# Kernel tuning notes

Measured on AMD Instinct MI355X. Metric: run time of the kernel, lower is better.

Reference implementation:

```python
import jax, jax.numpy as jnp
import numpy as np

V_PER_MESH = 6596
HIDDEN = 128
# per-body-part clamp limits from the original module (parts 1..14)
LIMITS = jnp.array([0.04, 0.06, 0.04, 0.04, 0.02, 0.02, 0.04, 0.04,
                    0.03, 0.03, 0.02, 0.02, 0.01, 0.01], dtype=jnp.float32)


def setup_inputs() -> dict:
    key = jax.random.key(0)
    ks = jax.random.split(key, 16)
    B, V, H = 32, V_PER_MESH, HIDDEN
    N = B * V
    E = 3 * N
    inp = {}
    inp["verts"] = jax.random.normal(ks[0], (N, 3), jnp.float32)
    inp["normals"] = jax.random.normal(ks[1], (N, 3), jnp.float32)
    inp["anchor_v"] = jax.random.uniform(ks[2], (V, 3), jnp.float32)
    inp["edges"] = jax.random.randint(ks[3], (E, 2), 0, N)
    inp["part_id"] = jax.random.randint(ks[4], (V,), 0, 14)
    dims = [3, H + 3, H + 3]  # first gconv sees only vert normals (vert_feat_dim=0)
    i = 5
    for l, d in enumerate(dims):
        s = 1.0 / np.sqrt(d)
        inp[f"w0_{l}"] = jax.random.normal(ks[i], (d, H), jnp.float32) * s; i += 1
        inp[f"b0_{l}"] = jnp.zeros((H,), jnp.float32)
        inp[f"w1_{l}"] = jax.random.normal(ks[i], (d, H), jnp.float32) * s; i += 1
        inp[f"b1_{l}"] = jnp.zeros((H,), jnp.float32)
    inp["w_off"] = jax.random.normal(ks[i], (H + 3, 3), jnp.float32) * 0.01
    inp["b_off"] = jnp.zeros((3,), jnp.float32)
    return inp


def _forward(verts, normals, anchor_v, edges, part_id, layers, w_off, b_off):
    N = verts.shape[0]
    B = N // V_PER_MESH
    e0, e1 = edges[:, 0], edges[:, 1]
    feats = normals  # vert_pos_packed (verts_normals_packed), vert_feats=None
    for (w0, b0, w1, b1) in layers:
        x0 = feats @ w0 + b0            # [N,H] self transform
        x1 = feats @ w1 + b1            # [N,H] neighbor transform
        # undirected gather-scatter over mesh edges
        nbr = jnp.zeros_like(x0).at[e0].add(x1[e1]).at[e1].add(x1[e0])
        h = jax.nn.relu(x0 + nbr)       # vert_feats_nopos
        feats = jnp.concatenate([h, normals], axis=1)  # [N,H+3]
    deform = jnp.tanh(feats @ w_off + b_off)  # [N,3]
    # per-body-part clamp, vectorized: one limit per vertex, tiled over meshes
    lim = jnp.tile(LIMITS[part_id], B)[:, None]          # [N,1]
    clamped = jnp.clip(deform, -lim, lim)
    anchor = jnp.tile(anchor_v, (B, 1))                  # [N,3]
    new_verts = verts + clamped * anchor                 # offset_verts
    return new_verts, h


def reference(verts, normals, anchor_v, edges, part_id,
              w0_0, b0_0, w1_0, b1_0,
              w0_1, b0_1, w1_1, b1_1,
              w0_2, b0_2, w1_2, b1_2,
              w_off, b_off):
    layers = [(w0_0, b0_0, w1_0, b1_0),
              (w0_1, b0_1, w1_1, b1_1),
              (w0_2, b0_2, w1_2, b1_2)]
    return _forward(verts, normals, anchor_v, edges, part_id, layers, w_off, b_off)
```

## Files before the change

### kernel.cpp

```cpp
#include <hip/hip_runtime.h>

#define N_TOT 211072
#define V_MESH 6596
#define E_TOT 633216
#define CAP 32
#define KD 264
#define KSTEPS 8

typedef __attribute__((ext_vector_type(8))) short bf16x8;
typedef __attribute__((ext_vector_type(4))) float f32x4;

__constant__ float c_LIM[14] = {0.04f,0.06f,0.04f,0.04f,0.02f,0.02f,0.04f,0.04f,
                                0.03f,0.03f,0.02f,0.02f,0.01f,0.01f};

__device__ __forceinline__ unsigned f2bf(float f) {
    unsigned x = __float_as_uint(f);
    return (x + 0x7fffu + ((x >> 16) & 1u)) >> 16;
}
__device__ __forceinline__ float bflo(unsigned u) { return __uint_as_float(u << 16); }
__device__ __forceinline__ float bfhi(unsigned u) { return __uint_as_float(u & 0xffff0000u); }
__device__ __forceinline__ unsigned cvt_pk_bf16(float lo, float hi) {
    unsigned r;
    asm("v_cvt_pk_bf16_f32 %0, %1, %2" : "=v"(r) : "v"(lo), "v"(hi));
    return r;
}

__global__ __launch_bounds__(256) void fill_adj_kernel(const int* __restrict__ edges,
                                                       int* __restrict__ cnt,
                                                       int* __restrict__ adj) {
    int e = blockIdx.x * 256 + threadIdx.x;
    if (e >= E_TOT) return;
    int2 ed = ((const int2*)edges)[e];
    int p0 = atomicAdd(&cnt[ed.x], 1);
    if (p0 < CAP) adj[(size_t)ed.x * CAP + p0] = ed.y;
    int p1 = atomicAdd(&cnt[ed.y], 1);
    if (p1 < CAP) adj[(size_t)ed.y * CAP + p1] = ed.x;
}

__global__ __launch_bounds__(256) void prep_nrm4_kernel(const float* __restrict__ normals,
                                                        float4* __restrict__ nrm4) {
    int i = blockIdx.x * 256 + threadIdx.x;
    if (i >= N_TOT) return;
    float4 v;
    v.x = normals[(size_t)i * 3 + 0];
    v.y = normals[(size_t)i * 3 + 1];
    v.z = normals[(size_t)i * 3 + 2];
    v.w = 0.f;
    nrm4[i] = v;
}

__global__ __launch_bounds__(256) void nsum_kernel(const float4* __restrict__ nrm4,
                                                   const int* __restrict__ cnt,
                                                   const int* __restrict__ adj,
                                                   float4* __restrict__ SS) {
    int i = blockIdx.x * 256 + threadIdx.x;
    if (i >= N_TOT) return;
    int deg = cnt[i]; if (deg > CAP) deg = CAP;
    const int4* a4 = (const int4*)(adj + (size_t)i * CAP);
    int4 A = a4[0], B = a4[1];
    float4 n0 = nrm4[A.x], n1 = nrm4[A.y], n2 = nrm4[A.z], n3 = nrm4[A.w];
    float4 m0 = nrm4[B.x], m1 = nrm4[B.y], m2 = nrm4[B.z], m3 = nrm4[B.w];
    float sx = ((n0.x + n1.x) + (n2.x + n3.x)) + ((m0.x + m1.x) + (m2.x + m3.x));
    float sy = ((n0.y + n1.y) + (n2.y + n3.y)) + ((m0.y + m1.y) + (m2.y + m3.y));
    float sz = ((n0.z + n1.z) + (n2.z + n3.z)) + ((m0.z + m1.z) + (m2.z + m3.z));
    for (int bq = 8; bq < deg; bq += 8) {
        int4 C = a4[bq / 4], D = a4[bq / 4 + 1];
        float4 p0 = nrm4[C.x], p1 = nrm4[C.y], p2 = nrm4[C.z], p3 = nrm4[C.w];
        float4 q0 = nrm4[D.x], q1 = nrm4[D.y], q2 = nrm4[D.z], q3 = nrm4[D.w];
        sx += ((p0.x + p1.x) + (p2.x + p3.x)) + ((q0.x + q1.x) + (q2.x + q3.x));
        sy += ((p0.y + p1.y) + (p2.y + p3.y)) + ((q0.y + q1.y) + (q2.y + q3.y));
        sz += ((p0.z + p1.z) + (p2.z + p3.z)) + ((q0.z + q1.z) + (q2.z + q3.z));
    }
    float4 out; out.x = sx; out.y = sy; out.z = sz; out.w = (float)deg;
    SS[i] = out;
}

__global__ __launch_bounds__(256) void conv_w2_kernel(const float* __restrict__ w0,
                                                      const float* __restrict__ b0,
                                                      const float* __restrict__ w1,
                                                      const float* __restrict__ b1,
                                                      short* __restrict__ Wt,
                                                      float4* __restrict__ hdA,
                                                      float4* __restrict__ hdB) {
    int c = blockIdx.x;
    for (int k = threadIdx.x; k < KD; k += 256) {
        unsigned val = 0u;
        if (k < 128)      val = f2bf(w0[(size_t)k * 128 + c]);
        else if (k < 256) val = f2bf(w1[(size_t)(k - 128) * 128 + c]);
        Wt[(size_t)c * KD + k] = (short)val;
    }
    if (threadIdx.x == 0) {
        hdA[c] = make_float4(b0[c], b1[c], w0[128 * 128 + c], w0[129 * 128 + c]);
        hdB[c] = make_float4(w0[130 * 128 + c], w1[128 * 128 + c],
                             w1[129 * 128 + c], w1[130 * 128 + c]);
    }
}

__global__ __launch_bounds__(1024) void fused1_kernel(const float4* __restrict__ nrm4,
                                                      const float4* __restrict__ SS,
                                                      const float* __restrict__ w0,
                                                      const float* __restrict__ b0,
                                                      const float* __restrict__ w1,
                                                      const float* __restrict__ b1,
                                                      unsigned* __restrict__ hout) {
    __shared__ float wL[2][3][128];
    __shared__ float bL[2][128];
    int tid  = threadIdx.x;
    int w    = tid >> 6;
    int lane = tid & 63;
    int i    = blockIdx.x * 16 + w;

    if (tid < 768) {
        int mm = tid / 384, r = tid - mm * 384;
        (&wL[mm][0][0])[r] = (mm ? w1 : w0)[r];
    } else if (tid < 1024) {
        int t2 = tid - 768;
        if (t2 < 256) bL[t2 >> 7][t2 & 127] = ((t2 >> 7) ? b1 : b0)[t2 & 127];
    }
    float4 self4 = nrm4[i];
    float4 S4 = SS[i];
    float degf = S4.w;
    __syncthreads();

    int c0 = 2 * lane, c1 = 2 * lane + 1;
    float h0 = bL[0][c0] + degf * bL[1][c0]
             + self4.x * wL[0][0][c0] + self4.y * wL[0][1][c0] + self4.z * wL[0][2][c0]
             + S4.x * wL[1][0][c0] + S4.y * wL[1][1][c0] + S4.z * wL[1][2][c0];
    float h1 = bL[0][c1] + degf * bL[1][c1]
             + self4.x * wL[0][0][c1] + self4.y * wL[0][1][c1] + self4.z * wL[0][2][c1]
             + S4.x * wL[1][0][c1] + S4.y * wL[1][1][c1] + S4.z * wL[1][2][c1];
    hout[(size_t)i * 64 + lane] = cvt_pk_bf16(fmaxf(h0, 0.f), fmaxf(h1, 0.f));
}

template<int LAST>
__global__ __launch_bounds__(512, 6) void fused2_kernel(const unsigned* __restrict__ hin,
                                                        const float4* __restrict__ nrm4,
                                                        const float4* __restrict__ SS,
                                                        const int* __restrict__ cnt,
                                                        const int* __restrict__ adj,
                                                        const short* __restrict__ Wt,
                                                        const float4* __restrict__ hdA,
                                                        const float4* __restrict__ hdB,
                                                        unsigned* __restrict__ hnext,
                                                        const float* __restrict__ verts,
                                                        const float* __restrict__ anchor_v,
                                                        const int* __restrict__ part_id,
                                                        const float* __restrict__ w_off,
                                                        const float* __restrict__ b_off,
                                                        float* __restrict__ houtf,
                                                        float* __restrict__ out_verts) {
    __shared__ short tileA[16 * KD];
    __shared__ unsigned tileC[16 * 64];
    __shared__ float headL[16][8];
    __shared__ float woL[131 * 3];
    __shared__ float partL[8][16][3];

    int tid  = threadIdx.x;
    int w    = tid >> 6;
    int lane = tid & 63;
    int g    = lane >> 4;
    int ln   = lane & 15;
    int row0 = blockIdx.x * 16;
    int rA   = 2 * w, rB = 2 * w + 1;
    int iA   = row0 + rA, iB = row0 + rB;

    if (LAST) {
        for (int t = tid; t < 131 * 3; t += 512) woL[t] = w_off[t];
    }

    int node = (lane < 32) ? iA : iB;
    int jv = adj[(size_t)node * CAP + (lane & 31)];
    int degA = cnt[iA]; degA = (degA > CAP) ? CAP : degA;
    int degB = cnt[iB]; degB = (degB > CAP) ? CAP : degB;
    unsigned selfA = hin[(size_t)iA * 64 + lane];
    unsigned selfB = hin[(size_t)iB * 64 + lane];
    float4 nn = nrm4[node];
    float4 sv = SS[node];
    if ((lane & 31) == 0) {
        int r = rA + (lane >> 5);
        headL[r][0] = nn.x; headL[r][1] = nn.y; headL[r][2] = nn.z; headL[r][3] = sv.w;
        headL[r][4] = sv.x; headL[r][5] = sv.y; headL[r][6] = sv.z; headL[r][7] = 0.f;
    }

    const unsigned* hb = hin + lane;
    unsigned uA[16], uB[16];
    #pragma unroll
    for (int q = 0; q < 16; ++q) {
        int jA = __builtin_amdgcn_readlane(jv, q);
        uA[q] = hb[(ptrdiff_t)jA * 64];
    }
    #pragma unroll
    for (int q = 0; q < 16; ++q) {
        int jB = __builtin_amdgcn_readlane(jv, 32 + q);
        uB[q] = hb[(ptrdiff_t)jB * 64];
    }
    float sA0 = 0.f, sA1 = 0.f, sB0 = 0.f, sB1 = 0.f;
    #pragma unroll
    for (int q = 0; q < 16; ++q) { sA0 += bflo(uA[q]); sA1 += bfhi(uA[q]); }
    #pragma unroll
    for (int q = 0; q < 16; ++q) { sB0 += bflo(uB[q]); sB1 += bfhi(uB[q]); }

    degA = __builtin_amdgcn_readfirstlane(degA);
    degB = __builtin_amdgcn_readfirstlane(degB);
    int degM = (degA > degB) ? degA : degB;
    for (int bq = 16; bq < degM; bq += 8) {
        unsigned vA[8], vB[8];
        #pragma unroll
        for (int q = 0; q < 8; ++q) {
            int jA = __builtin_amdgcn_readlane(jv, bq + q);
            int jB = __builtin_amdgcn_readlane(jv, 32 + bq + q);
            vA[q] = hb[(ptrdiff_t)jA * 64];
            vB[q] = hb[(ptrdiff_t)jB * 64];
        }
        #pragma unroll
        for (int q = 0; q < 8; ++q) {
            sA0 += bflo(vA[q]); sA1 += bfhi(vA[q]);
            sB0 += bflo(vB[q]); sB1 += bfhi(vB[q]);
        }
    }

    unsigned* tA = (unsigned*)tileA;
    tA[rA * 132 + lane]      = selfA;
    tA[rB * 132 + lane]      = selfB;
    tA[rA * 132 + 64 + lane] = cvt_pk_bf16(sA0, sA1);
    tA[rB * 132 + 64 + lane] = cvt_pk_bf16(sB0, sB1);
    if (lane < 4) {
        tA[rA * 132 + 128 + lane] = 0u;
        tA[rB * 132 + 128 + lane] = 0u;
    }

    int cb = w * 16, c = cb + ln;
    bf16x8 bfrag[KSTEPS];
    #pragma unroll
    for (int kk = 0; kk < KSTEPS; ++kk)
        bfrag[kk] = *(const bf16x8*)(Wt + (size_t)c * KD + kk * 32 + g * 8);
    float4 hA = hdA[c], hB = hdB[c];
    __syncthreads();

    f32x4 acc;
    #pragma unroll
    for (int j = 0; j < 4; ++j) {
        int r = g * 4 + j;
        acc[j] = hA.x + headL[r][3] * hA.y
               + headL[r][0] * hA.z + headL[r][1] * hA.w + headL[r][2] * hB.x
               + headL[r][4] * hB.y + headL[r][5] * hB.z + headL[r][6] * hB.w;
    }
    #pragma unroll
    for (int kk = 0; kk < KSTEPS; ++kk) {
        bf16x8 af = *(const bf16x8*)(tileA + ln * KD + kk * 32 + g * 8);
        acc = __builtin_amdgcn_mfma_f32_16x16x32_bf16(af, bfrag[kk], acc, 0, 0, 0);
    }
    #pragma unroll
    for (int j = 0; j < 4; ++j) acc[j] = fmaxf(acc[j], 0.f);

    if (!LAST) {
        #pragma unroll
        for (int j = 0; j < 4; ++j) {
            float po = __shfl_xor(acc[j], 1);
            if (!(ln & 1)) {
                unsigned pk = cvt_pk_bf16(acc[j], po);
                int r = g * 4 + j;
                int d = (cb + ln) >> 1;
                tileC[r * 64 + (d ^ ((r & 12) << 1))] = pk;
            }
        }
        __syncthreads();
        int r2 = 2 * w + (lane >> 5);
        int d2 = (lane & 31) * 2;
        int key = (r2 & 12) << 1;
        uint2 v2 = *(const uint2*)&tileC[r2 * 64 + (d2 ^ key)];
        *(uint2*)(hnext + (size_t)(row0 + r2) * 64 + d2) = v2;
    } else {
        #pragma unroll
        for (int j = 0; j < 4; ++j) {
            int r = g * 4 + j;
            float p0 = acc[j] * woL[c * 3 + 0];
            float p1 = acc[j] * woL[c * 3 + 1];
            float p2 = acc[j] * woL[c * 3 + 2];
            #pragma unroll
            for (int d = 1; d < 16; d <<= 1) {
                p0 += __shfl_xor(p0, d);
                p1 += __shfl_xor(p1, d);
                p2 += __shfl_xor(p2, d);
            }
            if (ln == 0) {
                partL[w][r][0] = p0; partL[w][r][1] = p1; partL[w][r][2] = p2;
            }
        }
        __syncthreads();
        float* tCf = (float*)tileA;
        #pragma unroll
        for (int j = 0; j < 4; ++j) {
            int r = g * 4 + j;
            tCf[r * 132 + c] = acc[j];
        }
        __syncthreads();
        {
            int r = tid >> 5, c4 = (tid & 31) * 4;
            float4 v = *(const float4*)&tCf[r * 132 + c4];
            *(float4*)(houtf + (size_t)(row0 + r) * 128 + c4) = v;
        }
        if (tid < 48) {
            int r = tid / 3, t = tid - r * 3;
            int i = row0 + r;
            float s = 0.f;
            #pragma unroll
            for (int ww = 0; ww < 8; ++ww) s += partL[ww][r][t];
            s += headL[r][0] * woL[128 * 3 + t] + headL[r][1] * woL[129 * 3 + t]
               + headL[r][2] * woL[130 * 3 + t] + b_off[t];
            float dd = tanhf(s);
            int v = i % V_MESH;
            float lim = c_LIM[part_id[v]];
            dd = fminf(fmaxf(dd, -lim), lim);
            out_verts[(size_t)i * 3 + t] =
                verts[(size_t)i * 3 + t] + dd * anchor_v[(size_t)v * 3 + t];
        }
    }
}

extern "C" void kernel_launch(void* const* d_in, const int* in_sizes, int n_in,
                              void* d_out, int out_size, void* d_ws, size_t ws_size,
                              hipStream_t stream) {
    const float* verts    = (const float*)d_in[0];
    const float* normals  = (const float*)d_in[1];
    const float* anchor_v = (const float*)d_in[2];
    const int*   edges    = (const int*)d_in[3];
    const int*   part_id  = (const int*)d_in[4];
    const float* w0_0 = (const float*)d_in[5];
    const float* b0_0 = (const float*)d_in[6];
    const float* w1_0 = (const float*)d_in[7];
    const float* b1_0 = (const float*)d_in[8];
    const float* w0_1 = (const float*)d_in[9];
    const float* b0_1 = (const float*)d_in[10];
    const float* w1_1 = (const float*)d_in[11];
    const float* b1_1 = (const float*)d_in[12];
    const float* w0_2 = (const float*)d_in[13];
    const float* b0_2 = (const float*)d_in[14];
    const float* w1_2 = (const float*)d_in[15];
    const float* b1_2 = (const float*)d_in[16];
    const float* w_off = (const float*)d_in[17];
    const float* b_off = (const float*)d_in[18];

    float* out_verts = (float*)d_out;
    float* houtf = (float*)d_out + (size_t)3 * N_TOT;

    char* p = (char*)d_ws;
    unsigned* h1b = (unsigned*)p;  p += (size_t)(N_TOT + 1) * 64 * 4;
    unsigned* h2b = (unsigned*)p;  p += (size_t)(N_TOT + 1) * 64 * 4;
    int*    cnt  = (int*)p;        p += (size_t)N_TOT * 4;
    int*    adj  = (int*)p;        p += (size_t)N_TOT * CAP * 4;
    short*  Wt1  = (short*)p;      p += 128 * KD * 2;
    short*  Wt2  = (short*)p;      p += 128 * KD * 2;
    float4* hdA1 = (float4*)p;     p += 128 * 16;
    float4* hdB1 = (float4*)p;     p += 128 * 16;
    float4* hdA2 = (float4*)p;     p += 128 * 16;
    float4* hdB2 = (float4*)p;     p += 128 * 16;
    float4* nrm4b = (float4*)p;    p += (size_t)(N_TOT + 1) * 16;
    float4* SS   = (float4*)p;     p += (size_t)N_TOT * 16;

    unsigned* h1 = h1b + 64;
    unsigned* h2 = h2b + 64;
    float4* nrm4 = nrm4b + 1;

    hipMemsetAsync(cnt, 0, (size_t)N_TOT * 4, stream);
    hipMemsetAsync(h1b, 0, 256, stream);
    hipMemsetAsync(h2b, 0, 256, stream);
    hipMemsetAsync(nrm4b, 0, 16, stream);
    hipMemsetAsync(adj, 0xFF, (size_t)N_TOT * CAP * 4, stream);
    fill_adj_kernel<<<(E_TOT + 255) / 256, 256, 0, stream>>>(edges, cnt, adj);
    prep_nrm4_kernel<<<(N_TOT + 255) / 256, 256, 0, stream>>>(normals, nrm4);
    conv_w2_kernel<<<128, 256, 0, stream>>>(w0_1, b0_1, w1_1, b1_1, Wt1, hdA1, hdB1);
    conv_w2_kernel<<<128, 256, 0, stream>>>(w0_2, b0_2, w1_2, b1_2, Wt2, hdA2, hdB2);
    nsum_kernel<<<(N_TOT + 255) / 256, 256, 0, stream>>>(nrm4, cnt, adj, SS);

    fused1_kernel<<<N_TOT / 16, 1024, 0, stream>>>(nrm4, SS, w0_0, b0_0, w1_0, b1_0, h1);
    fused2_kernel<0><<<N_TOT / 16, 512, 0, stream>>>(h1, nrm4, SS, cnt, adj, Wt1, hdA1, hdB1,
                                                     h2, nullptr, nullptr, nullptr, nullptr,
                                                     nullptr, nullptr, nullptr);
    fused2_kernel<1><<<N_TOT / 16, 512, 0, stream>>>(h2, nrm4, SS, cnt, adj, Wt2, hdA2, hdB2,
                                                     nullptr, verts, anchor_v, part_id,
                                                     w_off, b_off, houtf, out_verts);
}
```

Before: 412.4 us.

## Merge setup kernels and memsets into one init kernel, tune gather kernel

Five memsets and three small prep kernels (normals padding, two weight conversions) become a single init kernel, which removes launch and memset overhead. In the gather kernel the first neighbour batch shrinks from 16 to 8 per node, with the loop continuing from 8. Degree now comes from SS.w instead of a separate cnt load, and launch bounds rise to 8 waves per EU. Output stores become nontemporal and the weight-fragment loads move after the barrier, which may increase register pressure under the tighter occupancy bound.

```diff
diff --git a/kernel.cpp b/kernel.cpp
--- a/kernel.cpp
+++ b/kernel.cpp
@@ -9,6 +9,7 @@
 
 typedef __attribute__((ext_vector_type(8))) short bf16x8;
 typedef __attribute__((ext_vector_type(4))) float f32x4;
+typedef __attribute__((ext_vector_type(2))) unsigned u32x2;
 
 __constant__ float c_LIM[14] = {0.04f,0.06f,0.04f,0.04f,0.02f,0.02f,0.04f,0.04f,
                                 0.03f,0.03f,0.02f,0.02f,0.01f,0.01f};
@@ -23,6 +24,56 @@
     unsigned r;
     asm("v_cvt_pk_bf16_f32 %0, %1, %2" : "=v"(r) : "v"(lo), "v"(hi));
     return r;
+}
+
+__global__ __launch_bounds__(256) void init_kernel(const float* __restrict__ normals,
+                                                   const float* __restrict__ w0_1,
+                                                   const float* __restrict__ b0_1,
+                                                   const float* __restrict__ w1_1,
+                                                   const float* __restrict__ b1_1,
+                                                   const float* __restrict__ w0_2,
+                                                   const float* __restrict__ b0_2,
+                                                   const float* __restrict__ w1_2,
+                                                   const float* __restrict__ b1_2,
+                                                   int* __restrict__ cnt,
+                                                   int4* __restrict__ adj4,
+                                                   unsigned* __restrict__ h1b,
+                                                   unsigned* __restrict__ h2b,
+                                                   float4* __restrict__ nrm4b,
+                                                   short* __restrict__ Wt1,
+                                                   float4* __restrict__ hdA1,
+                                                   float4* __restrict__ hdB1,
+                                                   short* __restrict__ Wt2,
+                                                   float4* __restrict__ hdA2,
+                                                   float4* __restrict__ hdB2) {
+    unsigned idx = blockIdx.x * 256 + threadIdx.x;
+    if (idx < (unsigned)(N_TOT * CAP / 4)) adj4[idx] = make_int4(-1, -1, -1, -1);
+    if (idx < (unsigned)N_TOT) {
+        cnt[idx] = 0;
+        float4 v;
+        v.x = normals[(size_t)idx * 3 + 0];
+        v.y = normals[(size_t)idx * 3 + 1];
+        v.z = normals[(size_t)idx * 3 + 2];
+        v.w = 0.f;
+        nrm4b[idx + 1] = v;
+    }
+    if (idx == 0) nrm4b[0] = make_float4(0.f, 0.f, 0.f, 0.f);
+    if (idx < 64) { h1b[idx] = 0u; h2b[idx] = 0u; }
+    if (idx < (unsigned)(128 * KD)) {
+        int c = idx / KD, k = idx - c * KD;
+        unsigned v1 = 0u, v2 = 0u;
+        if (k < 128)      { v1 = f2bf(w0_1[(size_t)k * 128 + c]);        v2 = f2bf(w0_2[(size_t)k * 128 + c]); }
+        else if (k < 256) { v1 = f2bf(w1_1[(size_t)(k - 128) * 128 + c]); v2 = f2bf(w1_2[(size_t)(k - 128) * 128 + c]); }
+        Wt1[idx] = (short)v1;
+        Wt2[idx] = (short)v2;
+    }
+    if (idx < 128) {
+        int c = idx;
+        hdA1[c] = make_float4(b0_1[c], b1_1[c], w0_1[128*128 + c], w0_1[129*128 + c]);
+        hdB1[c] = make_float4(w0_1[130*128 + c], w1_1[128*128 + c], w1_1[129*128 + c], w1_1[130*128 + c]);
+        hdA2[c] = make_float4(b0_2[c], b1_2[c], w0_2[128*128 + c], w0_2[129*128 + c]);
+        hdB2[c] = make_float4(w0_2[130*128 + c], w1_2[128*128 + c], w1_2[129*128 + c], w1_2[130*128 + c]);
+    }
 }
 
 __global__ __launch_bounds__(256) void fill_adj_kernel(const int* __restrict__ edges,
@@ -35,18 +86,6 @@
     if (p0 < CAP) adj[(size_t)ed.x * CAP + p0] = ed.y;
     int p1 = atomicAdd(&cnt[ed.y], 1);
     if (p1 < CAP) adj[(size_t)ed.y * CAP + p1] = ed.x;
-}
-
-__global__ __launch_bounds__(256) void prep_nrm4_kernel(const float* __restrict__ normals,
-                                                        float4* __restrict__ nrm4) {
-    int i = blockIdx.x * 256 + threadIdx.x;
-    if (i >= N_TOT) return;
-    float4 v;
-    v.x = normals[(size_t)i * 3 + 0];
-    v.y = normals[(size_t)i * 3 + 1];
-    v.z = normals[(size_t)i * 3 + 2];
-    v.w = 0.f;
-    nrm4[i] = v;
 }
 
 __global__ __launch_bounds__(256) void nsum_kernel(const float4* __restrict__ nrm4,
@@ -75,27 +114,6 @@
     SS[i] = out;
 }
 
-__global__ __launch_bounds__(256) void conv_w2_kernel(const float* __restrict__ w0,
-                                                      const float* __restrict__ b0,
-                                                      const float* __restrict__ w1,
-                                                      const float* __restrict__ b1,
-                                                      short* __restrict__ Wt,
-                                                      float4* __restrict__ hdA,
-                                                      float4* __restrict__ hdB) {
-    int c = blockIdx.x;
-    for (int k = threadIdx.x; k < KD; k += 256) {
-        unsigned val = 0u;
-        if (k < 128)      val = f2bf(w0[(size_t)k * 128 + c]);
-        else if (k < 256) val = f2bf(w1[(size_t)(k - 128) * 128 + c]);
-        Wt[(size_t)c * KD + k] = (short)val;
-    }
-    if (threadIdx.x == 0) {
-        hdA[c] = make_float4(b0[c], b1[c], w0[128 * 128 + c], w0[129 * 128 + c]);
-        hdB[c] = make_float4(w0[130 * 128 + c], w1[128 * 128 + c],
-                             w1[129 * 128 + c], w1[130 * 128 + c]);
-    }
-}
-
 __global__ __launch_bounds__(1024) void fused1_kernel(const float4* __restrict__ nrm4,
                                                       const float4* __restrict__ SS,
                                                       const float* __restrict__ w0,
@@ -133,10 +151,9 @@
 }
 
 template<int LAST>
-__global__ __launch_bounds__(512, 6) void fused2_kernel(const unsigned* __restrict__ hin,
+__global__ __launch_bounds__(512, 8) void fused2_kernel(const unsigned* __restrict__ hin,
                                                         const float4* __restrict__ nrm4,
                                                         const float4* __restrict__ SS,
-                                                        const int* __restrict__ cnt,
                                                         const int* __restrict__ adj,
                                                         const short* __restrict__ Wt,
                                                         const float4* __restrict__ hdA,
@@ -170,12 +187,11 @@
 
     int node = (lane < 32) ? iA : iB;
     int jv = adj[(size_t)node * CAP + (lane & 31)];
-    int degA = cnt[iA]; degA = (degA > CAP) ? CAP : degA;
-    int degB = cnt[iB]; degB = (degB > CAP) ? CAP : degB;
     unsigned selfA = hin[(size_t)iA * 64 + lane];
     unsigned selfB = hin[(size_t)iB * 64 + lane];
     float4 nn = nrm4[node];
     float4 sv = SS[node];
+    int degl = (int)sv.w;
     if ((lane & 31) == 0) {
         int r = rA + (lane >> 5);
         headL[r][0] = nn.x; headL[r][1] = nn.y; headL[r][2] = nn.z; headL[r][3] = sv.w;
@@ -183,27 +199,24 @@
     }
 
     const unsigned* hb = hin + lane;
-    unsigned uA[16], uB[16];
-    #pragma unroll
-    for (int q = 0; q < 16; ++q) {
+    unsigned uA[8], uB[8];
+    #pragma unroll
+    for (int q = 0; q < 8; ++q) {
         int jA = __builtin_amdgcn_readlane(jv, q);
+        int jB = __builtin_amdgcn_readlane(jv, 32 + q);
         uA[q] = hb[(ptrdiff_t)jA * 64];
-    }
-    #pragma unroll
-    for (int q = 0; q < 16; ++q) {
-        int jB = __builtin_amdgcn_readlane(jv, 32 + q);
         uB[q] = hb[(ptrdiff_t)jB * 64];
     }
     float sA0 = 0.f, sA1 = 0.f, sB0 = 0.f, sB1 = 0.f;
     #pragma unroll
-    for (int q = 0; q < 16; ++q) { sA0 += bflo(uA[q]); sA1 += bfhi(uA[q]); }
-    #pragma unroll
-    for (int q = 0; q < 16; ++q) { sB0 += bflo(uB[q]); sB1 += bfhi(uB[q]); }
-
-    degA = __builtin_amdgcn_readfirstlane(degA);
-    degB = __builtin_amdgcn_readfirstlane(degB);
+    for (int q = 0; q < 8; ++q) {
+        sA0 += bflo(uA[q]); sA1 += bfhi(uA[q]);
+        sB0 += bflo(uB[q]); sB1 += bfhi(uB[q]);
+    }
+    int degA = __builtin_amdgcn_readlane(degl, 0);
+    int degB = __builtin_amdgcn_readlane(degl, 32);
     int degM = (degA > degB) ? degA : degB;
-    for (int bq = 16; bq < degM; bq += 8) {
+    for (int bq = 8; bq < degM; bq += 8) {
         unsigned vA[8], vB[8];
         #pragma unroll
         for (int q = 0; q < 8; ++q) {
@@ -228,14 +241,14 @@
         tA[rA * 132 + 128 + lane] = 0u;
         tA[rB * 132 + 128 + lane] = 0u;
     }
+    __syncthreads();
 
     int cb = w * 16, c = cb + ln;
+    float4 hA = hdA[c], hB = hdB[c];
     bf16x8 bfrag[KSTEPS];
     #pragma unroll
     for (int kk = 0; kk < KSTEPS; ++kk)
         bfrag[kk] = *(const bf16x8*)(Wt + (size_t)c * KD + kk * 32 + g * 8);
-    float4 hA = hdA[c], hB = hdB[c];
-    __syncthreads();
 
     f32x4 acc;
     #pragma unroll
@@ -268,8 +281,8 @@
         int r2 = 2 * w + (lane >> 5);
         int d2 = (lane & 31) * 2;
         int key = (r2 & 12) << 1;
-        uint2 v2 = *(const uint2*)&tileC[r2 * 64 + (d2 ^ key)];
-        *(uint2*)(hnext + (size_t)(row0 + r2) * 64 + d2) = v2;
+        u32x2 v2 = *(const u32x2*)&tileC[r2 * 64 + (d2 ^ key)];
+        __builtin_nontemporal_store(v2, (u32x2*)(hnext + (size_t)(row0 + r2) * 64 + d2));
     } else {
         #pragma unroll
         for (int j = 0; j < 4; ++j) {
@@ -297,8 +310,8 @@
         __syncthreads();
         {
             int r = tid >> 5, c4 = (tid & 31) * 4;
-            float4 v = *(const float4*)&tCf[r * 132 + c4];
-            *(float4*)(houtf + (size_t)(row0 + r) * 128 + c4) = v;
+            f32x4 v = *(const f32x4*)&tCf[r * 132 + c4];
+            __builtin_nontemporal_store(v, (f32x4*)(houtf + (size_t)(row0 + r) * 128 + c4));
         }
         if (tid < 48) {
             int r = tid / 3, t = tid - r * 3;
@@ -362,22 +375,17 @@
     unsigned* h2 = h2b + 64;
     float4* nrm4 = nrm4b + 1;
 
-    hipMemsetAsync(cnt, 0, (size_t)N_TOT * 4, stream);
-    hipMemsetAsync(h1b, 0, 256, stream);
-    hipMemsetAsync(h2b, 0, 256, stream);
-    hipMemsetAsync(nrm4b, 0, 16, stream);
-    hipMemsetAsync(adj, 0xFF, (size_t)N_TOT * CAP * 4, stream);
+    init_kernel<<<(N_TOT * CAP / 4 + 255) / 256, 256, 0, stream>>>(
+        normals, w0_1, b0_1, w1_1, b1_1, w0_2, b0_2, w1_2, b1_2,
+        cnt, (int4*)adj, h1b, h2b, nrm4b, Wt1, hdA1, hdB1, Wt2, hdA2, hdB2);
     fill_adj_kernel<<<(E_TOT + 255) / 256, 256, 0, stream>>>(edges, cnt, adj);
-    prep_nrm4_kernel<<<(N_TOT + 255) / 256, 256, 0, stream>>>(normals, nrm4);
-    conv_w2_kernel<<<128, 256, 0, stream>>>(w0_1, b0_1, w1_1, b1_1, Wt1, hdA1, hdB1);
-    conv_w2_kernel<<<128, 256, 0, stream>>>(w0_2, b0_2, w1_2, b1_2, Wt2, hdA2, hdB2);
     nsum_kernel<<<(N_TOT + 255) / 256, 256, 0, stream>>>(nrm4, cnt, adj, SS);
 
     fused1_kernel<<<N_TOT / 16, 1024, 0, stream>>>(nrm4, SS, w0_0, b0_0, w1_0, b1_0, h1);
-    fused2_kernel<0><<<N_TOT / 16, 512, 0, stream>>>(h1, nrm4, SS, cnt, adj, Wt1, hdA1, hdB1,
+    fused2_kernel<0><<<N_TOT / 16, 512, 0, stream>>>(h1, nrm4, SS, adj, Wt1, hdA1, hdB1,
                                                      h2, nullptr, nullptr, nullptr, nullptr,
                                                      nullptr, nullptr, nullptr);
-    fused2_kernel<1><<<N_TOT / 16, 512, 0, stream>>>(h2, nrm4, SS, cnt, adj, Wt2, hdA2, hdB2,
+    fused2_kernel<1><<<N_TOT / 16, 512, 0, stream>>>(h2, nrm4, SS, adj, Wt2, hdA2, hdB2,
                                                      nullptr, verts, anchor_v, part_id,
                                                      w_off, b_off, houtf, out_verts);
 }
```

Result: faster. 392.8 us (-4.7%).
